# Kernel optimization log

Hardware: AMD Instinct MI355X
Metric: run time of the kernel (lower is better)

## Reference

```python
import math
import jax, jax.numpy as jnp
import numpy as np

HEADS = 8
DIM = 512
HEAD_SIZE = DIM // HEADS  # 64


def setup_inputs() -> dict:
    key = jax.random.key(0)
    ks = jax.random.split(key, 5)
    b, nh, nw, t, d = 16, 16, 16, 16, DIM
    x = jax.random.normal(ks[0], (b, nh, nw, t, d), dtype=jnp.float32)
    s = 1.0 / math.sqrt(d)
    Wq = jax.random.normal(ks[1], (d, d), dtype=jnp.float32) * s
    Wk = jax.random.normal(ks[2], (d, d), dtype=jnp.float32) * s
    Wv = jax.random.normal(ks[3], (d, d), dtype=jnp.float32) * s
    Wo = jax.random.normal(ks[4], (d, d), dtype=jnp.float32) * s
    z = jnp.zeros((d,), dtype=jnp.float32)
    return {"x": x, "Wq": Wq, "bq": z, "Wk": Wk, "bk": z, "Wv": Wv, "bv": z, "Wo": Wo, "bo": z}


def _split_heads(t):
    # [b, n1, n2, T, D] -> [b, n1, n2, H, T, hs]
    b, n1, n2, T, _ = t.shape
    return t.reshape(b, n1, n2, T, HEADS, HEAD_SIZE).transpose(0, 1, 2, 4, 3, 5)


def reference(x, Wq, bq, Wk, bk, Wv, bv, Wo, bo):
    q = _split_heads(x @ Wq + bq)
    k = _split_heads(x @ Wk + bk)
    v = _split_heads(x @ Wv + bv)
    # windowed attention scores: [b, n1, n2, H, T, T]
    scores = jnp.einsum('bnmhtd,bnmhsd->bnmhts', q, k) / math.sqrt(HEAD_SIZE)
    probs = jax.nn.sigmoid(scores)  # NOTE: elementwise sigmoid, not softmax
    ctx = jnp.einsum('bnmhts,bnmhsd->bnmhtd', probs, v)
    b, n1, n2, H, T, hs = ctx.shape
    ctx = ctx.transpose(0, 1, 2, 4, 3, 5).reshape(b, n1, n2, T, H * hs)
    return ctx @ Wo + bo
```

## Files before the change

kernel.cpp:

```cpp
#include <hip/hip_runtime.h>
#include <hip/hip_bf16.h>

typedef float f32x4 __attribute__((ext_vector_type(4)));
typedef __bf16 bf16x8 __attribute__((ext_vector_type(8)));
typedef unsigned short u16x4 __attribute__((ext_vector_type(4)));
typedef unsigned short u16x8 __attribute__((ext_vector_type(8)));

__device__ __forceinline__ unsigned short f2bf(float f) {
  union { float f; unsigned u; } x; x.f = f;
  unsigned r = x.u + 0x7FFFu + ((x.u >> 16) & 1u);
  return (unsigned short)(r >> 16);
}
__device__ __forceinline__ float bf2f(unsigned short u) {
  union { unsigned u; float f; } x; x.u = ((unsigned)u) << 16;
  return x.f;
}

__device__ __forceinline__ void gl16(const void* g, void* l) {
  __builtin_amdgcn_global_load_lds(
      (const __attribute__((address_space(1))) unsigned*)g,
      (__attribute__((address_space(3))) unsigned*)l, 16, 0, 0);
}

__global__ __launch_bounds__(256) void prep_wt(const float* __restrict__ Wq,
                                               const float* __restrict__ Wk,
                                               const float* __restrict__ Wv,
                                               const float* __restrict__ Wo,
                                               unsigned short* __restrict__ WT) {
  __shared__ unsigned short ts[64][65];
  const float* W = (blockIdx.z == 0) ? Wq : (blockIdx.z == 1) ? Wk
                   : (blockIdx.z == 2) ? Wv : Wo;
  const int t = threadIdx.x;
  const int kbase = blockIdx.y * 64;
  const int nbase = blockIdx.x * 64;
  for (int i = 0; i < 16; ++i) {
    int idx = i * 256 + t;
    int r = idx >> 6, c = idx & 63;
    ts[r][c] = f2bf(W[(size_t)(kbase + r) * 512 + nbase + c]);
  }
  __syncthreads();
  unsigned short* dst = WT + (size_t)blockIdx.z * 512 * 512;
  for (int i = 0; i < 16; ++i) {
    int idx = i * 256 + t;
    int nn = idx >> 6, kk = idx & 63;
    dst[(size_t)(nbase + nn) * 512 + kbase + kk] = ts[kk][nn];
  }
}

__global__ void prep_bias(const float* __restrict__ bq, const float* __restrict__ bk,
                          const float* __restrict__ bv, float* __restrict__ biasc) {
  int i = blockIdx.x * 256 + threadIdx.x;
  if (i < 512) biasc[i] = bq[i];
  else if (i < 1024) biasc[i] = bk[i - 512];
  else if (i < 1536) biasc[i] = bv[i - 1024];
}

__global__ __launch_bounds__(256) void convert_x(const float* __restrict__ x,
                                                 unsigned short* __restrict__ xb,
                                                 long long n8) {
  long long i = (long long)blockIdx.x * 256 + threadIdx.x;
  const long long stride = (long long)gridDim.x * 256;
  for (; i < n8; i += stride) {
    f32x4 a = *reinterpret_cast<const f32x4*>(&x[i * 8]);
    f32x4 b = *reinterpret_cast<const f32x4*>(&x[i * 8 + 4]);
    u16x8 o;
    o[0] = f2bf(a[0]); o[1] = f2bf(a[1]); o[2] = f2bf(a[2]); o[3] = f2bf(a[3]);
    o[4] = f2bf(b[0]); o[5] = f2bf(b[1]); o[6] = f2bf(b[2]); o[7] = f2bf(b[3]);
    *reinterpret_cast<u16x8*>(&xb[i * 8]) = o;
  }
}

template <typename CT>
__global__ __launch_bounds__(512, 2) void gemm256(
    const unsigned short* __restrict__ A, int lda,
    const unsigned short* __restrict__ BT,
    CT* __restrict__ C, int ldc,
    const float* __restrict__ bias, int NB) {
  __shared__ alignas(16) unsigned short pool[66048];
  const int t = threadIdx.x;
  const int lane = t & 63;
  const int w = t >> 6;
  const int wm = w >> 2, wn = w & 3;

  const int nwg = gridDim.x;
  const int cpx = nwg >> 3;
  const int wg = (blockIdx.x & 7) * cpx + (blockIdx.x >> 3);
  const int n0 = (wg % NB) * 256;
  const int m0 = (wg / NB) * 256;

  const int sr = lane >> 3;
  const int sg = ((lane & 7) ^ sr) << 3;
  const unsigned short* gA = A + (size_t)(m0 + w * 8 + sr) * lda + sg;
  const unsigned short* gB = BT + (size_t)(n0 + w * 8 + sr) * 512 + sg;
  const int lw = w * 512;

#define STAGE_A(kt, h, b)                                                   \
  { const unsigned short* g_ = gA + (size_t)(h) * 128 * lda + (kt) * 64;    \
    unsigned short* l_ = &pool[(b) * 16384 + (h) * 8192 + lw];              \
    gl16(g_, l_); gl16(g_ + (size_t)64 * lda, l_ + 4096); }
#define STAGE_B(kt, h, b)                                                   \
  { const unsigned short* g_ = gB + (size_t)(h) * 128 * 512 + (kt) * 64;    \
    unsigned short* l_ = &pool[32768 + (b) * 16384 + (h) * 8192 + lw];      \
    gl16(g_, l_); gl16(g_ + (size_t)64 * 512, l_ + 4096); }

  const int fr = lane & 15;
  const int fg = lane >> 4;
  const int fx = lane & 7;
  auto readA = [&](int b, int mi, int kf) -> bf16x8 {
    return *reinterpret_cast<const bf16x8*>(
        &pool[(b) * 16384 + (wm * 128 + mi * 16 + fr) * 64 +
              ((((kf << 2) + fg) ^ fx) << 3)]);
  };
  auto readB = [&](int b, int ni, int kf) -> bf16x8 {
    return *reinterpret_cast<const bf16x8*>(
        &pool[32768 + (b) * 16384 + (wn * 64 + ni * 16 + fr) * 64 +
              ((((kf << 2) + fg) ^ fx) << 3)]);
  };

  f32x4 acc[8][4];
#pragma unroll
  for (int i = 0; i < 8; ++i)
#pragma unroll
    for (int j = 0; j < 4; ++j) acc[i][j] = (f32x4){0.f, 0.f, 0.f, 0.f};
  bf16x8 bfr[4][2];

#define PHASE(b, q, READB, STAGES, VM)                                       \
  {                                                                          \
    bf16x8 a0_ = readA(b, 2 * (q), 0), a1_ = readA(b, 2 * (q), 1);           \
    bf16x8 a2_ = readA(b, 2 * (q) + 1, 0), a3_ = readA(b, 2 * (q) + 1, 1);   \
    if (READB) {                                                             \
      _Pragma("unroll") for (int ni = 0; ni < 4; ++ni) {                     \
        bfr[ni][0] = readB(b, ni, 0);                                        \
        bfr[ni][1] = readB(b, ni, 1);                                        \
      }                                                                      \
    }                                                                        \
    STAGES;                                                                  \
    if ((VM) == 4) asm volatile("s_waitcnt vmcnt(4)" ::: "memory");          \
    if ((VM) == 0) asm volatile("s_waitcnt vmcnt(0)" ::: "memory");          \
    __builtin_amdgcn_s_barrier();                                            \
    asm volatile("s_waitcnt lgkmcnt(0)" ::: "memory");                       \
    __builtin_amdgcn_sched_barrier(0);                                       \
    __builtin_amdgcn_s_setprio(1);                                           \
    _Pragma("unroll") for (int ni = 0; ni < 4; ++ni) {                       \
      acc[2 * (q)][ni] = __builtin_amdgcn_mfma_f32_16x16x32_bf16(            \
          a0_, bfr[ni][0], acc[2 * (q)][ni], 0, 0, 0);                       \
      acc[2 * (q) + 1][ni] = __builtin_amdgcn_mfma_f32_16x16x32_bf16(        \
          a2_, bfr[ni][0], acc[2 * (q) + 1][ni], 0, 0, 0);                   \
    }                                                                        \
    _Pragma("unroll") for (int ni = 0; ni < 4; ++ni) {                       \
      acc[2 * (q)][ni] = __builtin_amdgcn_mfma_f32_16x16x32_bf16(            \
          a1_, bfr[ni][1], acc[2 * (q)][ni], 0, 0, 0);                       \
      acc[2 * (q) + 1][ni] = __builtin_amdgcn_mfma_f32_16x16x32_bf16(        \
          a3_, bfr[ni][1], acc[2 * (q) + 1][ni], 0, 0, 0);                   \
    }                                                                        \
    __builtin_amdgcn_s_setprio(0);                                           \
    __builtin_amdgcn_s_barrier();                                            \
  }

  STAGE_B(0, 0, 0); STAGE_B(0, 1, 0);
  STAGE_A(0, 0, 0); STAGE_A(0, 1, 0);
  STAGE_B(1, 0, 1); STAGE_B(1, 1, 1);
  asm volatile("s_waitcnt vmcnt(4)" ::: "memory");
  __builtin_amdgcn_s_barrier();

#pragma unroll
  for (int i = 0; i < 4; ++i) {
    const bool s2 = (i < 3);
    const int vmA = s2 ? 4 : 0;
    const int vmB = s2 ? 4 : 0;
    PHASE(0, 0, true,  { STAGE_A(2 * i + 1, 0, 1) }, -1);
    PHASE(0, 1, false, { STAGE_A(2 * i + 1, 1, 1) if (s2) STAGE_B(2 * i + 2, 0, 0) }, -1);
    PHASE(0, 2, false, { if (s2) STAGE_B(2 * i + 2, 1, 0) }, -1);
    PHASE(0, 3, false, {}, vmA);
    PHASE(1, 0, true,  { if (s2) STAGE_A(2 * i + 2, 0, 0) }, -1);
    PHASE(1, 1, false, { if (s2) STAGE_A(2 * i + 2, 1, 0) }, -1);
    PHASE(1, 2, false, { if (s2) STAGE_B(2 * i + 3, 0, 1) }, -1);
    PHASE(1, 3, false, { if (s2) STAGE_B(2 * i + 3, 1, 1) }, vmB);
  }
#undef PHASE
#undef STAGE_A
#undef STAGE_B

  __syncthreads();
  if constexpr (sizeof(CT) == 2) {
#pragma unroll
    for (int ni = 0; ni < 4; ++ni) {
      int cl = wn * 64 + ni * 16 + fr;
      float bc = bias[n0 + cl];
#pragma unroll
      for (int mi = 0; mi < 8; ++mi) {
        int rl = wm * 128 + mi * 16 + fg * 4;
#pragma unroll
        for (int r = 0; r < 4; ++r)
          pool[(rl + r) * 258 + cl] = f2bf(acc[mi][ni][r] + bc);
      }
    }
    __syncthreads();
#pragma unroll
    for (int it = 0; it < 16; ++it) {
      int idx = it * 512 + t;
      int row = idx >> 5, c8 = idx & 31;
      u16x8 v = *reinterpret_cast<const u16x8*>(&pool[row * 258 + c8 * 8]);
      *reinterpret_cast<u16x8*>(&C[(size_t)(m0 + row) * ldc + n0 + c8 * 8]) = v;
    }
  } else {
    float* stf = reinterpret_cast<float*>(pool);
#pragma unroll
    for (int h = 0; h < 2; ++h) {
      if (wm == h) {
#pragma unroll
        for (int ni = 0; ni < 4; ++ni) {
          int cl = wn * 64 + ni * 16 + fr;
          float bc = bias[n0 + cl];
#pragma unroll
          for (int mi = 0; mi < 8; ++mi) {
            int rl = mi * 16 + fg * 4;
#pragma unroll
            for (int r = 0; r < 4; ++r)
              stf[(rl + r) * 258 + cl] = acc[mi][ni][r] + bc;
          }
        }
      }
      __syncthreads();
#pragma unroll
      for (int it = 0; it < 16; ++it) {
        int idx = it * 512 + t;
        int row = idx >> 6, c4 = idx & 63;
        f32x4 v = *reinterpret_cast<const f32x4*>(&stf[row * 258 + c4 * 4]);
        *reinterpret_cast<f32x4*>(
            &C[(size_t)(m0 + h * 128 + row) * ldc + n0 + c4 * 4]) = v;
      }
      __syncthreads();
    }
  }
}

__global__ __launch_bounds__(256) void attn_kernel(unsigned short* __restrict__ QKV) {
  __shared__ alignas(16) unsigned short qs[16][1544];
  __shared__ unsigned short ps[8][16][16];
  const int t = threadIdx.x;
  const size_t base = (size_t)blockIdx.x * 16;

  {
    int row = t >> 4;
    int cb = (t & 15) * 96;
    const unsigned short* src = QKV + (base + row) * 1536;
#pragma unroll
    for (int i = 0; i < 24; ++i) {
      int c = cb + i * 4;
      *reinterpret_cast<u16x4*>(&qs[row][c]) = *reinterpret_cast<const u16x4*>(&src[c]);
    }
  }
  __syncthreads();

  const int tq = t >> 4;
  const int tk = t & 15;
#pragma unroll
  for (int h = 0; h < 8; ++h) {
    float acc = 0.f;
#pragma unroll
    for (int dc = 0; dc < 64; dc += 8) {
      u16x8 q8 = *reinterpret_cast<const u16x8*>(&qs[tq][h * 64 + dc]);
      u16x8 k8 = *reinterpret_cast<const u16x8*>(&qs[tk][512 + h * 64 + dc]);
#pragma unroll
      for (int j = 0; j < 8; ++j) acc += bf2f(q8[j]) * bf2f(k8[j]);
    }
    ps[h][tq][tk] = f2bf(1.0f / (1.0f + __expf(-acc * 0.125f)));
  }
  __syncthreads();

  const int row = t >> 4;
  const int cb4 = (t & 15) * 4;
  unsigned short* dst = QKV + (base + row) * 1536 + 1024;
#pragma unroll
  for (int h = 0; h < 8; ++h) {
    f32x4 acc = (f32x4){0.f, 0.f, 0.f, 0.f};
#pragma unroll
    for (int s = 0; s < 16; ++s) {
      float p = bf2f(ps[h][row][s]);
      u16x4 v4 = *reinterpret_cast<const u16x4*>(&qs[s][1024 + h * 64 + cb4]);
      acc[0] += p * bf2f(v4[0]); acc[1] += p * bf2f(v4[1]);
      acc[2] += p * bf2f(v4[2]); acc[3] += p * bf2f(v4[3]);
    }
    u16x4 o4;
    o4[0] = f2bf(acc[0]); o4[1] = f2bf(acc[1]); o4[2] = f2bf(acc[2]); o4[3] = f2bf(acc[3]);
    *reinterpret_cast<u16x4*>(&dst[h * 64 + cb4]) = o4;
  }
}

extern "C" void kernel_launch(void* const* d_in, const int* in_sizes, int n_in,
                              void* d_out, int out_size, void* d_ws, size_t ws_size,
                              hipStream_t stream) {
  const float* x  = (const float*)d_in[0];
  const float* Wq = (const float*)d_in[1];
  const float* bq = (const float*)d_in[2];
  const float* Wk = (const float*)d_in[3];
  const float* bk = (const float*)d_in[4];
  const float* Wv = (const float*)d_in[5];
  const float* bv = (const float*)d_in[6];
  const float* Wo = (const float*)d_in[7];
  const float* bo = (const float*)d_in[8];
  float* out = (float*)d_out;

  const int M = 65536;
  char* ws = (char*)d_ws;
  unsigned short* WT = (unsigned short*)ws;
  float* biasc = (float*)(ws + (size_t)2048 * 512 * 2);
  const long long prep_bytes = (long long)2048 * 512 * 2 + 8192;

  prep_wt<<<dim3(8, 8, 4), 256, 0, stream>>>(Wq, Wk, Wv, Wo, WT);
  prep_bias<<<6, 256, 0, stream>>>(bq, bk, bv, biasc);

  long long avail = (long long)ws_size - prep_bytes;
  int chunk_rows = 65536;
  while (chunk_rows > 2048 && (long long)chunk_rows * 4096 > avail) chunk_rows >>= 1;
  const int nchunks = M / chunk_rows;

  unsigned short* Xb  = (unsigned short*)(ws + prep_bytes);
  unsigned short* QKV = Xb + (size_t)chunk_rows * 512;

  for (int c = 0; c < nchunks; ++c) {
    const size_t row0 = (size_t)c * chunk_rows;
    const int mt = chunk_rows / 256;
    convert_x<<<2048, 256, 0, stream>>>(x + row0 * 512, Xb,
                                        (long long)chunk_rows * 64);
    gemm256<unsigned short><<<mt * 6, 512, 0, stream>>>(
        Xb, 512, WT, QKV, 1536, biasc, 6);
    attn_kernel<<<chunk_rows / 16, 256, 0, stream>>>(QKV);
    gemm256<float><<<mt * 2, 512, 0, stream>>>(
        QKV + 1024, 1536, WT + (size_t)1536 * 512, out + row0 * 512, 512, bo, 2);
  }
}
```

Baseline: 302.7 us.

## Rewrite windowed sigmoid attention with MFMA and double-buffered async K/V loads

Replaces the scalar-FMA attention kernel with one that computes QK^T and PV using bf16 MFMA 16x16x32 instructions. Each block handles 128 rows (8 windows), and K/V tiles for the next head are prefetched into swizzled LDS via global_load_lds while the current head is computed. Q fragments are read straight from global memory. The aim is to cut ALU-bound scalar dot products and raise throughput. The cost is extra complexity: strided LDS gathers for the V fragments and in-place writes of the context over the V region.

```diff
diff --git a/kernel.cpp b/kernel.cpp
--- a/kernel.cpp
+++ b/kernel.cpp
@@ -10,10 +10,6 @@
   union { float f; unsigned u; } x; x.f = f;
   unsigned r = x.u + 0x7FFFu + ((x.u >> 16) & 1u);
   return (unsigned short)(r >> 16);
-}
-__device__ __forceinline__ float bf2f(unsigned short u) {
-  union { unsigned u; float f; } x; x.u = ((unsigned)u) << 16;
-  return x.f;
 }
 
 __device__ __forceinline__ void gl16(const void* g, void* l) {
@@ -235,57 +231,91 @@
   }
 }
 
-__global__ __launch_bounds__(256) void attn_kernel(unsigned short* __restrict__ QKV) {
-  __shared__ alignas(16) unsigned short qs[16][1544];
-  __shared__ unsigned short ps[8][16][16];
+__global__ __launch_bounds__(256) void attn2(unsigned short* __restrict__ QKV) {
+  __shared__ alignas(16) unsigned short sh[33792];
+  const int VS = 16384, PS = 32768;
   const int t = threadIdx.x;
-  const size_t base = (size_t)blockIdx.x * 16;
-
-  {
-    int row = t >> 4;
-    int cb = (t & 15) * 96;
-    const unsigned short* src = QKV + (base + row) * 1536;
-#pragma unroll
-    for (int i = 0; i < 24; ++i) {
-      int c = cb + i * 4;
-      *reinterpret_cast<u16x4*>(&qs[row][c]) = *reinterpret_cast<const u16x4*>(&src[c]);
-    }
-  }
+  const int lane = t & 63;
+  const int w = t >> 6;
+  const int fr = lane & 15, fg = lane >> 4, fx = lane & 7;
+  const int sr = lane >> 3;
+  const int sgx = ((lane & 7) ^ sr) << 3;
+  const int sgl = (lane & 7) << 3;
+  const size_t m0r = (size_t)blockIdx.x * 128;
+
+#define SK2(h, b)                                                            \
+  _Pragma("unroll") for (int u = 0; u < 4; ++u) {                            \
+    const int r0 = u * 32 + w * 8;                                           \
+    gl16(QKV + (m0r + r0 + sr) * 1536 + 512 + (h) * 64 + sgx,                \
+         &sh[(b) * 8192 + r0 * 64]);                                         \
+  }
+#define SV2(h, b)                                                            \
+  _Pragma("unroll") for (int u = 0; u < 4; ++u) {                            \
+    const int r0 = u * 32 + w * 8;                                           \
+    gl16(QKV + (m0r + r0 + sr) * 1536 + 1024 + (h) * 64 + sgl,               \
+         &sh[VS + (b) * 8192 + r0 * 64]);                                    \
+  }
+
+  SK2(0, 0) SV2(0, 0)
+  asm volatile("s_waitcnt vmcnt(0)" ::: "memory");
   __syncthreads();
 
-  const int tq = t >> 4;
-  const int tk = t & 15;
-#pragma unroll
   for (int h = 0; h < 8; ++h) {
-    float acc = 0.f;
-#pragma unroll
-    for (int dc = 0; dc < 64; dc += 8) {
-      u16x8 q8 = *reinterpret_cast<const u16x8*>(&qs[tq][h * 64 + dc]);
-      u16x8 k8 = *reinterpret_cast<const u16x8*>(&qs[tk][512 + h * 64 + dc]);
-#pragma unroll
-      for (int j = 0; j < 8; ++j) acc += bf2f(q8[j]) * bf2f(k8[j]);
-    }
-    ps[h][tq][tk] = f2bf(1.0f / (1.0f + __expf(-acc * 0.125f)));
-  }
-  __syncthreads();
-
-  const int row = t >> 4;
-  const int cb4 = (t & 15) * 4;
-  unsigned short* dst = QKV + (base + row) * 1536 + 1024;
-#pragma unroll
-  for (int h = 0; h < 8; ++h) {
-    f32x4 acc = (f32x4){0.f, 0.f, 0.f, 0.f};
-#pragma unroll
-    for (int s = 0; s < 16; ++s) {
-      float p = bf2f(ps[h][row][s]);
-      u16x4 v4 = *reinterpret_cast<const u16x4*>(&qs[s][1024 + h * 64 + cb4]);
-      acc[0] += p * bf2f(v4[0]); acc[1] += p * bf2f(v4[1]);
-      acc[2] += p * bf2f(v4[2]); acc[3] += p * bf2f(v4[3]);
-    }
-    u16x4 o4;
-    o4[0] = f2bf(acc[0]); o4[1] = f2bf(acc[1]); o4[2] = f2bf(acc[2]); o4[3] = f2bf(acc[3]);
-    *reinterpret_cast<u16x4*>(&dst[h * 64 + cb4]) = o4;
-  }
+    const int b = h & 1;
+    u16x8 q[2][2];
+#pragma unroll
+    for (int ww = 0; ww < 2; ++ww) {
+      const int wi = w * 2 + ww;
+      const unsigned short* qrow = QKV + (m0r + wi * 16 + fr) * 1536 + h * 64;
+      q[ww][0] = *reinterpret_cast<const u16x8*>(qrow + fg * 8);
+      q[ww][1] = *reinterpret_cast<const u16x8*>(qrow + 32 + fg * 8);
+    }
+    if (h < 7) { SK2(h + 1, b ^ 1) SV2(h + 1, b ^ 1) }
+
+#pragma unroll
+    for (int ww = 0; ww < 2; ++ww) {
+      const int wi = w * 2 + ww;
+      f32x4 s = (f32x4){0.f, 0.f, 0.f, 0.f};
+      {
+        bf16x8 kf_ = *reinterpret_cast<const bf16x8*>(
+            &sh[b * 8192 + (wi * 16 + fr) * 64 + ((fg ^ fx) << 3)]);
+        s = __builtin_amdgcn_mfma_f32_16x16x32_bf16(
+            kf_, __builtin_bit_cast(bf16x8, q[ww][0]), s, 0, 0, 0);
+        kf_ = *reinterpret_cast<const bf16x8*>(
+            &sh[b * 8192 + (wi * 16 + fr) * 64 + (((4 + fg) ^ fx) << 3)]);
+        s = __builtin_amdgcn_mfma_f32_16x16x32_bf16(
+            kf_, __builtin_bit_cast(bf16x8, q[ww][1]), s, 0, 0, 0);
+      }
+      u16x4 pfu;
+#pragma unroll
+      for (int r = 0; r < 4; ++r)
+        pfu[r] = f2bf(1.0f / (1.0f + __expf(-s[r] * 0.125f)));
+      *reinterpret_cast<u16x4*>(&sh[PS + w * 256 + fr * 16 + fg * 4]) = pfu;
+      u16x8 pbu = (u16x8){0, 0, 0, 0, 0, 0, 0, 0};
+      if (fg < 2)
+        pbu = *reinterpret_cast<const u16x8*>(&sh[PS + w * 256 + fr * 16 + fg * 8]);
+      bf16x8 pb = __builtin_bit_cast(bf16x8, pbu);
+#pragma unroll
+      for (int dc = 0; dc < 4; ++dc) {
+        u16x8 vau;
+#pragma unroll
+        for (int j = 0; j < 8; ++j)
+          vau[j] = sh[VS + b * 8192 + (wi * 16 + (fg & 1) * 8 + j) * 64 + dc * 16 + fr];
+        f32x4 c = __builtin_amdgcn_mfma_f32_16x16x32_bf16(
+            __builtin_bit_cast(bf16x8, vau), pb, (f32x4){0.f, 0.f, 0.f, 0.f},
+            0, 0, 0);
+        u16x4 o;
+#pragma unroll
+        for (int r = 0; r < 4; ++r) o[r] = f2bf(c[r]);
+        *reinterpret_cast<u16x4*>(
+            &QKV[(m0r + wi * 16 + fr) * 1536 + 1024 + h * 64 + dc * 16 + fg * 4]) = o;
+      }
+    }
+    asm volatile("s_waitcnt vmcnt(8)" ::: "memory");
+    __syncthreads();
+  }
+#undef SK2
+#undef SV2
 }
 
 extern "C" void kernel_launch(void* const* d_in, const int* in_sizes, int n_in,
@@ -326,7 +356,7 @@
                                         (long long)chunk_rows * 64);
     gemm256<unsigned short><<<mt * 6, 512, 0, stream>>>(
         Xb, 512, WT, QKV, 1536, biasc, 6);
-    attn_kernel<<<chunk_rows / 16, 256, 0, stream>>>(QKV);
+    attn2<<<chunk_rows / 128, 256, 0, stream>>>(QKV);
     gemm256<float><<<mt * 2, 512, 0, stream>>>(
         QKV + 1024, 1536, WT + (size_t)1536 * 512, out + row0 * 512, 512, bo, 2);
   }
```

Result: faster. 293.8 us (-3.0%).
